# Kernel tuning notes

Hardware: AMD Instinct MI355X
Metric: run time of the kernel (lower is better)

Reference implementation:

```python
import jax, jax.numpy as jnp
import numpy as np

D_MODEL = 512
DFF = 2048
E = 8
K = 2
B, N = 2, 2048


def setup_inputs() -> dict:
    key = jax.random.key(0)
    ks = jax.random.split(key, 6)
    x = jax.random.normal(ks[0], (B, N, D_MODEL), dtype=jnp.float32)
    # router: nn.Linear(d_model, E, bias=False), init normal(std=0.01), weight [E, d]
    router_w = jax.random.normal(ks[1], (E, D_MODEL), dtype=jnp.float32) * 0.01
    # expert linear1.weight [dff, d], linear2.weight [d, dff], xavier-uniform; biases zero in torch init,
    # but use small random biases so the backward test exercises their grads meaningfully.
    lim1 = float(np.sqrt(6.0 / (D_MODEL + DFF)))
    w1_all = jax.random.uniform(ks[2], (E, DFF, D_MODEL), minval=-lim1, maxval=lim1, dtype=jnp.float32)
    w2_all = jax.random.uniform(ks[3], (E, D_MODEL, DFF), minval=-lim1, maxval=lim1, dtype=jnp.float32)
    b1_all = jax.random.normal(ks[4], (E, DFF), dtype=jnp.float32) * 0.01
    b2_all = jax.random.normal(ks[5], (E, D_MODEL), dtype=jnp.float32) * 0.01
    return {"x": x, "router_w": router_w, "w1_all": w1_all, "b1_all": b1_all,
            "w2_all": w2_all, "b2_all": b2_all}


def reference(x, router_w, w1_all, b1_all, w2_all, b2_all):
    Bb, Nn, C = x.shape
    L = Bb * Nn
    x_flat = x.reshape(L, C)

    # Router: logits -> softmax -> top-k -> renormalized weights
    router_logits = x_flat @ router_w.T                      # [L, E]
    router_probs = jax.nn.softmax(router_logits, axis=-1)
    expert_weights, expert_indices = jax.lax.top_k(router_probs, K)  # [L, K]
    expert_weights = expert_weights / (jnp.sum(expert_weights, axis=-1, keepdims=True) + 1e-9)

    # Dense per-expert MLP (same math as per-token gathered bmm; dropout in eval = identity)
    h = jax.nn.relu(jnp.einsum('lc,efc->lef', x_flat, w1_all) + b1_all[None])  # [L, E, dff]
    out_all = jnp.einsum('lef,ecf->lec', h, w2_all) + b2_all[None]             # [L, E, C]

    # Gather selected experts' outputs and combine
    out_sel = jnp.take_along_axis(out_all, expert_indices[:, :, None], axis=1)  # [L, K, C]
    final = jnp.sum(out_sel * expert_weights[:, :, None], axis=1)               # [L, C]
    return final.reshape(Bb, Nn, C)
```

## Files before the change

kernel.cpp:

```cpp
#include <hip/hip_runtime.h>

#define D_MODEL 512
#define DFF 2048
#define NEXP 8
#define LTOK 4096
#define NPAIR 8192
#define PMAX 9216
#define MAXT 72

#define HD_COUNTS 0
#define HD_CURSOR 8
#define HD_OFF    16
#define HD_NTILES 25
#define HD_TILE_E 32
#define HD_TILE_R 112

typedef __attribute__((ext_vector_type(8))) short bf16x8;
typedef __attribute__((ext_vector_type(4))) float f32x4;

__device__ __forceinline__ unsigned short f2bf(float f){
  unsigned u = __builtin_bit_cast(unsigned, f);
  u += 0x7fffu + ((u>>16)&1u);
  return (unsigned short)(u>>16);
}

template<int N> __device__ __forceinline__ void wait_vm(){
  if constexpr (N==6)      asm volatile("s_waitcnt vmcnt(6)" ::: "memory");
  else                     asm volatile("s_waitcnt vmcnt(0)" ::: "memory");
}
#define RAW_BARRIER() asm volatile("s_barrier" ::: "memory")

__global__ void prep_kernel(const float* __restrict__ w1, const float* __restrict__ w2,
                            unsigned short* __restrict__ w1b, unsigned short* __restrict__ w2b,
                            const float* __restrict__ x, const float* __restrict__ rw,
                            int* __restrict__ pair_e, float* __restrict__ pair_w){
  int bx = blockIdx.x;
  int tid = threadIdx.x;
  if (bx < 8192){
    int id = bx*256 + tid;
    const int per = NEXP*DFF*D_MODEL/8;
    const float* src; unsigned short* dst; int k;
    if (id < per){ src = w1; dst = w1b; k = id; }
    else         { src = w2; dst = w2b; k = id - per; }
    const float4* s = (const float4*)(src + (size_t)k*8);
    float4 a = s[0], b = s[1];
    uint4 o;
    o.x = (unsigned)f2bf(a.x) | ((unsigned)f2bf(a.y)<<16);
    o.y = (unsigned)f2bf(a.z) | ((unsigned)f2bf(a.w)<<16);
    o.z = (unsigned)f2bf(b.x) | ((unsigned)f2bf(b.y)<<16);
    o.w = (unsigned)f2bf(b.z) | ((unsigned)f2bf(b.w)<<16);
    *(uint4*)(dst + (size_t)k*8) = o;
  } else {
    int t = (bx - 8192)*4 + (tid>>6);
    int l = tid & 63;
    const float* xr = x + (size_t)t*D_MODEL;
    float xv[8];
    #pragma unroll
    for (int j=0;j<8;j++) xv[j] = xr[j*64+l];
    double lg[NEXP];
    #pragma unroll
    for (int e=0;e<NEXP;e++){
      const float* we = rw + e*D_MODEL;
      double s = 0.0;
      #pragma unroll
      for (int j=0;j<8;j++) s += (double)xv[j] * (double)we[j*64+l];
      #pragma unroll
      for (int off=32; off; off>>=1) s += __shfl_xor(s, off);
      lg[e] = s;
    }
    if (l==0){
      double mx = lg[0];
      #pragma unroll
      for (int e=1;e<NEXP;e++) if (lg[e]>mx) mx = lg[e];
      double p[NEXP], sum = 0.0;
      #pragma unroll
      for (int e=0;e<NEXP;e++){ p[e] = exp(lg[e]-mx); sum += p[e]; }
      #pragma unroll
      for (int e=0;e<NEXP;e++) p[e] /= sum;
      int i0 = 0;
      for (int e=1;e<NEXP;e++) if (p[e] > p[i0]) i0 = e;
      int i1 = (i0==0) ? 1 : 0;
      for (int e=0;e<NEXP;e++){ if (e==i0) continue; if (p[e] > p[i1]) i1 = e; }
      double s2 = p[i0] + p[i1] + 1e-9;
      pair_e[2*t]   = i0;  pair_e[2*t+1] = i1;
      pair_w[2*t]   = (float)(p[i0]/s2);
      pair_w[2*t+1] = (float)(p[i1]/s2);
    }
  }
}

__global__ void count_kernel(const int* __restrict__ pair_e, int* __restrict__ hdr){
  __shared__ int cnt[NEXP];
  int tid = threadIdx.x;
  if (tid < NEXP) cnt[tid] = 0;
  __syncthreads();
  int base = blockIdx.x*1024;
  #pragma unroll
  for (int i=0;i<4;i++) atomicAdd(&cnt[pair_e[base + i*256 + tid]], 1);
  __syncthreads();
  if (tid < NEXP) atomicAdd(&hdr[HD_COUNTS+tid], cnt[tid]);
}

__global__ void plan_kernel(int* __restrict__ hdr, int* __restrict__ gtk){
  if (threadIdx.x==0){
    int off=0, nt=0;
    for (int e=0;e<NEXP;e++){
      hdr[HD_OFF+e]=off;
      int c = hdr[HD_COUNTS+e];
      int tiles = (c+127)>>7;
      for (int i=0;i<tiles;i++){ hdr[HD_TILE_E+nt]=e; hdr[HD_TILE_R+nt]=off+(i<<7); nt++; }
      off += tiles<<7;
    }
    hdr[HD_OFF+NEXP]=off;
    hdr[HD_NTILES]=nt;
  }
  for (int i=threadIdx.x; i<PMAX; i+=blockDim.x) gtk[i]=-1;
}

__global__ void assign_gather_kernel(const int* __restrict__ pair_e, int* __restrict__ hdr,
                                     int* __restrict__ gtk, const float* __restrict__ x,
                                     unsigned short* __restrict__ xg){
  __shared__ int cnt[NEXP];
  __shared__ int base[NEXP];
  __shared__ int rowbuf[256];
  int tid = threadIdx.x;
  if (tid < NEXP) cnt[tid] = 0;
  __syncthreads();
  int id = blockIdx.x*256 + tid;
  int e = pair_e[id];
  int myrank = atomicAdd(&cnt[e], 1);
  __syncthreads();
  if (tid < NEXP) base[tid] = atomicAdd(&hdr[HD_CURSOR+tid], cnt[tid]);
  __syncthreads();
  int row = hdr[HD_OFF+e] + base[e] + myrank;
  gtk[row] = id;
  rowbuf[tid] = row;
  __syncthreads();
  int grp = tid>>6, sub = tid&63;
  int base0 = blockIdx.x*256;
  for (int p = grp; p < 256; p += 4){
    int r = rowbuf[p];
    int t = (base0 + p)>>1;
    const float4* s = (const float4*)(x + (size_t)t*D_MODEL + sub*8);
    float4 a = s[0], b = s[1];
    uint4 o;
    o.x = (unsigned)f2bf(a.x) | ((unsigned)f2bf(a.y)<<16);
    o.y = (unsigned)f2bf(a.z) | ((unsigned)f2bf(a.w)<<16);
    o.z = (unsigned)f2bf(b.x) | ((unsigned)f2bf(b.y)<<16);
    o.w = (unsigned)f2bf(b.z) | ((unsigned)f2bf(b.w)<<16);
    *(uint4*)(xg + (size_t)r*D_MODEL + sub*8) = o;
  }
}

__global__ __launch_bounds__(512,2) void gemm1_k(
    const unsigned short* __restrict__ A,
    const unsigned short* __restrict__ Bw,
    const float* __restrict__ bias,
    unsigned short* __restrict__ outH,
    const int* __restrict__ hdr)
{
  constexpr int NWG = MAXT*8;
  __shared__ __align__(16) unsigned short As[2*128*64];
  __shared__ __align__(16) unsigned short Bs[2*256*64];

  int wg  = blockIdx.x;
  int swz = (wg & 7)*(NWG/8) + (wg >> 3);
  int m   = swz >> 3;
  int n0  = (swz & 7) << 8;

  if (m >= hdr[HD_NTILES]) return;
  int e    = hdr[HD_TILE_E+m];
  int row0 = hdr[HD_TILE_R+m];

  int tid = threadIdx.x;
  int w = tid>>6, l = tid&63;
  int wm = w>>2, wn = w&3;

  const unsigned short* Ag = A  + (size_t)row0*D_MODEL;
  const unsigned short* Bg = Bw + (size_t)e*DFF*D_MODEL + (size_t)n0*D_MODEL;

  f32x4 acc[4][4];
  f32x4 zz = {0.f,0.f,0.f,0.f};
  #pragma unroll
  for (int i=0;i<4;i++)
    #pragma unroll
    for (int j=0;j<4;j++) acc[i][j] = zz;

  int srow = (w<<3) + (l>>3);
  int c8   = l&7;
  char* AsB = (char*)As;
  char* BsB = (char*)Bs;

  auto stage = [&](int b, int kt){
    #pragma unroll
    for (int i=0;i<2;i++){
      int r  = i*64 + srow;
      int sc = (c8 ^ (r&7))*8;
      const unsigned short* ga = Ag + (size_t)r*D_MODEL + kt*64 + sc;
      int ldso = b*16384 + i*8192 + w*1024 + l*16;
      __builtin_amdgcn_global_load_lds((const __attribute__((address_space(1))) void*)ga,
                                       (__attribute__((address_space(3))) void*)(AsB + ldso), 16, 0, 0);
    }
    #pragma unroll
    for (int i=0;i<4;i++){
      int r  = i*64 + srow;
      int sc = (c8 ^ (r&7))*8;
      const unsigned short* gb = Bg + (size_t)r*D_MODEL + kt*64 + sc;
      int ldso = b*32768 + i*8192 + w*1024 + l*16;
      __builtin_amdgcn_global_load_lds((const __attribute__((address_space(1))) void*)gb,
                                       (__attribute__((address_space(3))) void*)(BsB + ldso), 16, 0, 0);
    }
  };

  auto compute = [&](int b){
    #pragma unroll
    for (int kk=0;kk<2;kk++){
      bf16x8 av[4], bv[4];
      #pragma unroll
      for (int mi=0;mi<4;mi++){
        int r  = (wm<<6) + (mi<<4) + (l&15);
        int ch = ((kk<<2) + (l>>4)) ^ (r&7);
        av[mi] = *(const bf16x8*)(AsB + b*16384 + r*128 + ch*16);
      }
      #pragma unroll
      for (int ni=0;ni<4;ni++){
        int r  = (wn<<6) + (ni<<4) + (l&15);
        int ch = ((kk<<2) + (l>>4)) ^ (r&7);
        bv[ni] = *(const bf16x8*)(BsB + b*32768 + r*128 + ch*16);
      }
      #pragma unroll
      for (int mi=0;mi<4;mi++)
        #pragma unroll
        for (int ni=0;ni<4;ni++)
          acc[mi][ni] = __builtin_amdgcn_mfma_f32_16x16x32_bf16(av[mi], bv[ni], acc[mi][ni], 0,0,0);
    }
  };

  stage(0, 0);
  int cur = 0;
  for (int kt=0; kt<D_MODEL/64-1; ++kt){
    stage(cur^1, kt+1);
    wait_vm<6>();
    RAW_BARRIER();
    compute(cur);
    asm volatile("s_waitcnt lgkmcnt(0)" ::: "memory");
    RAW_BARRIER();
    cur ^= 1;
  }
  wait_vm<0>();
  RAW_BARRIER();
  compute(cur);

  int lc = l&15, lq = l>>4;
  #pragma unroll
  for (int ni=0;ni<4;ni++){
    int col = n0 + (wn<<6) + (ni<<4) + lc;
    float bcol = bias[e*DFF + col];
    #pragma unroll
    for (int mi=0;mi<4;mi++){
      int rbase = row0 + (wm<<6) + (mi<<4) + lq*4;
      #pragma unroll
      for (int q=0;q<4;q++){
        float v = acc[mi][ni][q] + bcol;
        v = v>0.f ? v : 0.f;
        outH[(size_t)(rbase+q)*DFF + col] = f2bf(v);
      }
    }
  }
}

__global__ __launch_bounds__(256,3) void gemm2_k(
    const unsigned short* __restrict__ A,
    const unsigned short* __restrict__ Bw,
    const float* __restrict__ bias,
    float* __restrict__ outO,
    const float* __restrict__ pair_w,
    const int* __restrict__ hdr,
    const int* __restrict__ gtk)
{
  constexpr int NWG = 2*MAXT*4;
  __shared__ __align__(16) unsigned short As[2*64*64];
  __shared__ __align__(16) unsigned short Bs[2*128*64];

  int wg  = blockIdx.x;
  int swz = (wg & 7)*(NWG/8) + (wg >> 3);
  int m   = swz >> 2;
  int n0  = (swz & 3) << 7;

  if (m >= 2*hdr[HD_NTILES]) return;
  int e    = hdr[HD_TILE_E+(m>>1)];
  int row0 = hdr[HD_TILE_R+(m>>1)] + ((m&1)<<6);

  int tid = threadIdx.x;
  int w = tid>>6, l = tid&63;

  const unsigned short* Ag = A  + (size_t)row0*DFF;
  const unsigned short* Bg = Bw + (size_t)e*D_MODEL*DFF + (size_t)n0*DFF;

  f32x4 acc[4][2];
  f32x4 zz = {0.f,0.f,0.f,0.f};
  #pragma unroll
  for (int i=0;i<4;i++)
    #pragma unroll
    for (int j=0;j<2;j++) acc[i][j] = zz;

  int srow = (w<<3) + (l>>3);
  int c8   = l&7;
  char* AsB = (char*)As;
  char* BsB = (char*)Bs;

  auto stage = [&](int b, int kt){
    #pragma unroll
    for (int i=0;i<2;i++){
      int r  = i*32 + srow;
      int sc = (c8 ^ (r&7))*8;
      const unsigned short* ga = Ag + (size_t)r*DFF + kt*64 + sc;
      int ldso = b*8192 + i*4096 + w*1024 + l*16;
      __builtin_amdgcn_global_load_lds((const __attribute__((address_space(1))) void*)ga,
                                       (__attribute__((address_space(3))) void*)(AsB + ldso), 16, 0, 0);
    }
    #pragma unroll
    for (int i=0;i<4;i++){
      int r  = i*32 + srow;
      int sc = (c8 ^ (r&7))*8;
      const unsigned short* gb = Bg + (size_t)r*DFF + kt*64 + sc;
      int ldso = b*16384 + i*4096 + w*1024 + l*16;
      __builtin_amdgcn_global_load_lds((const __attribute__((address_space(1))) void*)gb,
                                       (__attribute__((address_space(3))) void*)(BsB + ldso), 16, 0, 0);
    }
  };

  auto compute = [&](int b){
    #pragma unroll
    for (int kk=0;kk<2;kk++){
      bf16x8 av[4], bv[2];
      #pragma unroll
      for (int mi=0;mi<4;mi++){
        int r  = (mi<<4) + (l&15);
        int ch = ((kk<<2) + (l>>4)) ^ (r&7);
        av[mi] = *(const bf16x8*)(AsB + b*8192 + r*128 + ch*16);
      }
      #pragma unroll
      for (int ni=0;ni<2;ni++){
        int r  = (w<<5) + (ni<<4) + (l&15);
        int ch = ((kk<<2) + (l>>4)) ^ (r&7);
        bv[ni] = *(const bf16x8*)(BsB + b*16384 + r*128 + ch*16);
      }
      #pragma unroll
      for (int mi=0;mi<4;mi++)
        #pragma unroll
        for (int ni=0;ni<2;ni++)
          acc[mi][ni] = __builtin_amdgcn_mfma_f32_16x16x32_bf16(av[mi], bv[ni], acc[mi][ni], 0,0,0);
    }
  };

  stage(0, 0);
  int cur = 0;
  for (int kt=0; kt<DFF/64-1; ++kt){
    stage(cur^1, kt+1);
    wait_vm<6>();
    RAW_BARRIER();
    compute(cur);
    asm volatile("s_waitcnt lgkmcnt(0)" ::: "memory");
    RAW_BARRIER();
    cur ^= 1;
  }
  wait_vm<0>();
  RAW_BARRIER();
  compute(cur);

  int lc = l&15, lq = l>>4;
  #pragma unroll
  for (int ni=0;ni<2;ni++){
    int col = n0 + (w<<5) + (ni<<4) + lc;
    float bcol = bias[e*D_MODEL + col];
    #pragma unroll
    for (int mi=0;mi<4;mi++){
      int rbase = row0 + (mi<<4) + lq*4;
      #pragma unroll
      for (int q=0;q<4;q++){
        int gr = rbase + q;
        float v = acc[mi][ni][q] + bcol;
        int tk = gtk[gr];
        if (tk>=0){
          float wgt = pair_w[tk];
          atomicAdd(&outO[(size_t)(tk>>1)*D_MODEL + col], wgt*v);
        }
      }
    }
  }
}

extern "C" void kernel_launch(void* const* d_in, const int* in_sizes, int n_in,
                              void* d_out, int out_size, void* d_ws, size_t ws_size,
                              hipStream_t stream){
  const float* x  = (const float*)d_in[0];
  const float* rw = (const float*)d_in[1];
  const float* w1 = (const float*)d_in[2];
  const float* b1 = (const float*)d_in[3];
  const float* w2 = (const float*)d_in[4];
  const float* b2 = (const float*)d_in[5];
  float* out = (float*)d_out;

  const size_t OFF_HDR  = 0;
  const size_t OFF_PE   = 1024;
  const size_t OFF_PW   = 66560;
  const size_t OFF_GTK  = 99328;
  const size_t OFF_XG   = 180224;
  const size_t OFF_W1B  = OFF_XG  + (size_t)PMAX*D_MODEL*2;
  const size_t OFF_W2B  = OFF_W1B + (size_t)NEXP*DFF*D_MODEL*2;
  const size_t OFF_H    = OFF_W2B + (size_t)NEXP*DFF*D_MODEL*2;
  const size_t WS_NEED  = OFF_H   + (size_t)PMAX*DFF*2;
  if (ws_size < WS_NEED) return;

  char* ws = (char*)d_ws;
  int*   hdr    = (int*)(ws + OFF_HDR);
  int*   pair_e = (int*)(ws + OFF_PE);
  float* pair_w = (float*)(ws + OFF_PW);
  int*   gtk    = (int*)(ws + OFF_GTK);
  unsigned short* xg  = (unsigned short*)(ws + OFF_XG);
  unsigned short* w1b = (unsigned short*)(ws + OFF_W1B);
  unsigned short* w2b = (unsigned short*)(ws + OFF_W2B);
  unsigned short* h   = (unsigned short*)(ws + OFF_H);

  hipMemsetAsync(hdr, 0, 1024, stream);
  hipMemsetAsync(out, 0, (size_t)LTOK*D_MODEL*sizeof(float), stream);
  prep_kernel<<<9216, 256, 0, stream>>>(w1, w2, w1b, w2b, x, rw, pair_e, pair_w);
  count_kernel<<<NPAIR/1024, 256, 0, stream>>>(pair_e, hdr);
  plan_kernel<<<1, 256, 0, stream>>>(hdr, gtk);
  assign_gather_kernel<<<NPAIR/256, 256, 0, stream>>>(pair_e, hdr, gtk, x, xg);
  gemm1_k<<<MAXT*8, 512, 0, stream>>>(xg, w1b, b1, h, hdr);
  gemm2_k<<<2*MAXT*4, 256, 0, stream>>>(h, w2b, b2, out, pair_w, hdr, gtk);
}
```

Baseline: 156.8 us.

## Triple-buffer GEMM K-loop prefetch and split router from weight conversion

```diff
diff --git a/kernel.cpp b/kernel.cpp
--- a/kernel.cpp
+++ b/kernel.cpp
@@ -25,68 +25,66 @@
 }
 
 template<int N> __device__ __forceinline__ void wait_vm(){
-  if constexpr (N==6)      asm volatile("s_waitcnt vmcnt(6)" ::: "memory");
+  if constexpr (N==12)     asm volatile("s_waitcnt vmcnt(12)" ::: "memory");
+  else if constexpr (N==6) asm volatile("s_waitcnt vmcnt(6)" ::: "memory");
   else                     asm volatile("s_waitcnt vmcnt(0)" ::: "memory");
 }
 #define RAW_BARRIER() asm volatile("s_barrier" ::: "memory")
 
-__global__ void prep_kernel(const float* __restrict__ w1, const float* __restrict__ w2,
-                            unsigned short* __restrict__ w1b, unsigned short* __restrict__ w2b,
-                            const float* __restrict__ x, const float* __restrict__ rw,
+__global__ void router_top2(const float* __restrict__ x, const float* __restrict__ rw,
                             int* __restrict__ pair_e, float* __restrict__ pair_w){
-  int bx = blockIdx.x;
-  int tid = threadIdx.x;
-  if (bx < 8192){
-    int id = bx*256 + tid;
-    const int per = NEXP*DFF*D_MODEL/8;
-    const float* src; unsigned short* dst; int k;
-    if (id < per){ src = w1; dst = w1b; k = id; }
-    else         { src = w2; dst = w2b; k = id - per; }
-    const float4* s = (const float4*)(src + (size_t)k*8);
-    float4 a = s[0], b = s[1];
-    uint4 o;
-    o.x = (unsigned)f2bf(a.x) | ((unsigned)f2bf(a.y)<<16);
-    o.y = (unsigned)f2bf(a.z) | ((unsigned)f2bf(a.w)<<16);
-    o.z = (unsigned)f2bf(b.x) | ((unsigned)f2bf(b.y)<<16);
-    o.w = (unsigned)f2bf(b.z) | ((unsigned)f2bf(b.w)<<16);
-    *(uint4*)(dst + (size_t)k*8) = o;
-  } else {
-    int t = (bx - 8192)*4 + (tid>>6);
-    int l = tid & 63;
-    const float* xr = x + (size_t)t*D_MODEL;
-    float xv[8];
-    #pragma unroll
-    for (int j=0;j<8;j++) xv[j] = xr[j*64+l];
-    double lg[NEXP];
-    #pragma unroll
-    for (int e=0;e<NEXP;e++){
-      const float* we = rw + e*D_MODEL;
-      double s = 0.0;
-      #pragma unroll
-      for (int j=0;j<8;j++) s += (double)xv[j] * (double)we[j*64+l];
-      #pragma unroll
-      for (int off=32; off; off>>=1) s += __shfl_xor(s, off);
-      lg[e] = s;
-    }
-    if (l==0){
-      double mx = lg[0];
-      #pragma unroll
-      for (int e=1;e<NEXP;e++) if (lg[e]>mx) mx = lg[e];
-      double p[NEXP], sum = 0.0;
-      #pragma unroll
-      for (int e=0;e<NEXP;e++){ p[e] = exp(lg[e]-mx); sum += p[e]; }
-      #pragma unroll
-      for (int e=0;e<NEXP;e++) p[e] /= sum;
-      int i0 = 0;
-      for (int e=1;e<NEXP;e++) if (p[e] > p[i0]) i0 = e;
-      int i1 = (i0==0) ? 1 : 0;
-      for (int e=0;e<NEXP;e++){ if (e==i0) continue; if (p[e] > p[i1]) i1 = e; }
-      double s2 = p[i0] + p[i1] + 1e-9;
-      pair_e[2*t]   = i0;  pair_e[2*t+1] = i1;
-      pair_w[2*t]   = (float)(p[i0]/s2);
-      pair_w[2*t+1] = (float)(p[i1]/s2);
-    }
-  }
+  int t = blockIdx.x;
+  int l = threadIdx.x;
+  const float* xr = x + (size_t)t*D_MODEL;
+  float xv[8];
+  #pragma unroll
+  for (int j=0;j<8;j++) xv[j] = xr[j*64+l];
+  double lg[NEXP];
+  #pragma unroll
+  for (int e=0;e<NEXP;e++){
+    const float* we = rw + e*D_MODEL;
+    double s = 0.0;
+    #pragma unroll
+    for (int j=0;j<8;j++) s += (double)xv[j] * (double)we[j*64+l];
+    #pragma unroll
+    for (int off=32; off; off>>=1) s += __shfl_xor(s, off);
+    lg[e] = s;
+  }
+  if (l==0){
+    double mx = lg[0];
+    #pragma unroll
+    for (int e=1;e<NEXP;e++) if (lg[e]>mx) mx = lg[e];
+    double p[NEXP], sum = 0.0;
+    #pragma unroll
+    for (int e=0;e<NEXP;e++){ p[e] = exp(lg[e]-mx); sum += p[e]; }
+    #pragma unroll
+    for (int e=0;e<NEXP;e++) p[e] /= sum;
+    int i0 = 0;
+    for (int e=1;e<NEXP;e++) if (p[e] > p[i0]) i0 = e;
+    int i1 = (i0==0) ? 1 : 0;
+    for (int e=0;e<NEXP;e++){ if (e==i0) continue; if (p[e] > p[i1]) i1 = e; }
+    double s2 = p[i0] + p[i1] + 1e-9;
+    pair_e[2*t]   = i0;  pair_e[2*t+1] = i1;
+    pair_w[2*t]   = (float)(p[i0]/s2);
+    pair_w[2*t+1] = (float)(p[i1]/s2);
+  }
+}
+
+__global__ void convw_kernel(const float* __restrict__ w1, const float* __restrict__ w2,
+                             unsigned short* __restrict__ w1b, unsigned short* __restrict__ w2b){
+  int id = blockIdx.x*256 + threadIdx.x;
+  const int per = NEXP*DFF*D_MODEL/8;
+  const float* src; unsigned short* dst; int k;
+  if (id < per){ src = w1; dst = w1b; k = id; }
+  else         { src = w2; dst = w2b; k = id - per; }
+  const float4* s = (const float4*)(src + (size_t)k*8);
+  float4 a = s[0], b = s[1];
+  uint4 o;
+  o.x = (unsigned)f2bf(a.x) | ((unsigned)f2bf(a.y)<<16);
+  o.y = (unsigned)f2bf(a.z) | ((unsigned)f2bf(a.w)<<16);
+  o.z = (unsigned)f2bf(b.x) | ((unsigned)f2bf(b.y)<<16);
+  o.w = (unsigned)f2bf(b.z) | ((unsigned)f2bf(b.w)<<16);
+  *(uint4*)(dst + (size_t)k*8) = o;
 }
 
 __global__ void count_kernel(const int* __restrict__ pair_e, int* __restrict__ hdr){
@@ -160,8 +158,9 @@
     const int* __restrict__ hdr)
 {
   constexpr int NWG = MAXT*8;
-  __shared__ __align__(16) unsigned short As[2*128*64];
-  __shared__ __align__(16) unsigned short Bs[2*256*64];
+  constexpr int NTK = D_MODEL/64;
+  __shared__ __align__(16) unsigned short As[3*128*64];
+  __shared__ __align__(16) unsigned short Bs[3*256*64];
 
   int wg  = blockIdx.x;
   int swz = (wg & 7)*(NWG/8) + (wg >> 3);
@@ -236,20 +235,18 @@
     }
   };
 
-  stage(0, 0);
-  int cur = 0;
-  for (int kt=0; kt<D_MODEL/64-1; ++kt){
-    stage(cur^1, kt+1);
-    wait_vm<6>();
+  stage(0,0); stage(1,1); stage(2,2);
+  for (int t=0; t<NTK; ++t){
+    if (t < NTK-2)       wait_vm<12>();
+    else if (t == NTK-2) wait_vm<6>();
+    else                 wait_vm<0>();
     RAW_BARRIER();
-    compute(cur);
+    int b = t%3;
+    compute(b);
     asm volatile("s_waitcnt lgkmcnt(0)" ::: "memory");
     RAW_BARRIER();
-    cur ^= 1;
-  }
-  wait_vm<0>();
-  RAW_BARRIER();
-  compute(cur);
+    if (t+3 < NTK) stage(b, t+3);
+  }
 
   int lc = l&15, lq = l>>4;
   #pragma unroll
@@ -269,7 +266,7 @@
   }
 }
 
-__global__ __launch_bounds__(256,3) void gemm2_k(
+__global__ __launch_bounds__(256,2) void gemm2_k(
     const unsigned short* __restrict__ A,
     const unsigned short* __restrict__ Bw,
     const float* __restrict__ bias,
@@ -279,8 +276,9 @@
     const int* __restrict__ gtk)
 {
   constexpr int NWG = 2*MAXT*4;
-  __shared__ __align__(16) unsigned short As[2*64*64];
-  __shared__ __align__(16) unsigned short Bs[2*128*64];
+  constexpr int NTK = DFF/64;
+  __shared__ __align__(16) unsigned short As[3*64*64];
+  __shared__ __align__(16) unsigned short Bs[3*128*64];
 
   int wg  = blockIdx.x;
   int swz = (wg & 7)*(NWG/8) + (wg >> 3);
@@ -354,20 +352,18 @@
     }
   };
 
-  stage(0, 0);
-  int cur = 0;
-  for (int kt=0; kt<DFF/64-1; ++kt){
-    stage(cur^1, kt+1);
-    wait_vm<6>();
+  stage(0,0); stage(1,1); stage(2,2);
+  for (int t=0; t<NTK; ++t){
+    if (t < NTK-2)       wait_vm<12>();
+    else if (t == NTK-2) wait_vm<6>();
+    else                 wait_vm<0>();
     RAW_BARRIER();
-    compute(cur);
+    int b = t%3;
+    compute(b);
     asm volatile("s_waitcnt lgkmcnt(0)" ::: "memory");
     RAW_BARRIER();
-    cur ^= 1;
-  }
-  wait_vm<0>();
-  RAW_BARRIER();
-  compute(cur);
+    if (t+3 < NTK) stage(b, t+3);
+  }
 
   int lc = l&15, lq = l>>4;
   #pragma unroll
@@ -425,7 +421,8 @@
 
   hipMemsetAsync(hdr, 0, 1024, stream);
   hipMemsetAsync(out, 0, (size_t)LTOK*D_MODEL*sizeof(float), stream);
-  prep_kernel<<<9216, 256, 0, stream>>>(w1, w2, w1b, w2b, x, rw, pair_e, pair_w);
+  router_top2<<<LTOK, 64, 0, stream>>>(x, rw, pair_e, pair_w);
+  convw_kernel<<<8192, 256, 0, stream>>>(w1, w2, w1b, w2b);
   count_kernel<<<NPAIR/1024, 256, 0, stream>>>(pair_e, hdr);
   plan_kernel<<<1, 256, 0, stream>>>(hdr, gtk);
   assign_gather_kernel<<<NPAIR/256, 256, 0, stream>>>(pair_e, hdr, gtk, x, xg);
```

Result: slower. 185.4 us (+18.2%).

## Enlarge expert row tiles to 256 and split-K gemm2 across wave groups

Applied to the files above, without the earlier changes.

```diff
diff --git a/kernel.cpp b/kernel.cpp
--- a/kernel.cpp
+++ b/kernel.cpp
@@ -5,8 +5,8 @@
 #define NEXP 8
 #define LTOK 4096
 #define NPAIR 8192
-#define PMAX 9216
-#define MAXT 72
+#define PMAX2 10240
+#define MAXT2 40
 
 #define HD_COUNTS 0
 #define HD_CURSOR 8
@@ -25,68 +25,66 @@
 }
 
 template<int N> __device__ __forceinline__ void wait_vm(){
-  if constexpr (N==6)      asm volatile("s_waitcnt vmcnt(6)" ::: "memory");
+  if constexpr (N==8)      asm volatile("s_waitcnt vmcnt(8)" ::: "memory");
+  else if constexpr (N==6) asm volatile("s_waitcnt vmcnt(6)" ::: "memory");
   else                     asm volatile("s_waitcnt vmcnt(0)" ::: "memory");
 }
 #define RAW_BARRIER() asm volatile("s_barrier" ::: "memory")
 
-__global__ void prep_kernel(const float* __restrict__ w1, const float* __restrict__ w2,
-                            unsigned short* __restrict__ w1b, unsigned short* __restrict__ w2b,
-                            const float* __restrict__ x, const float* __restrict__ rw,
+__global__ void router_top2(const float* __restrict__ x, const float* __restrict__ rw,
                             int* __restrict__ pair_e, float* __restrict__ pair_w){
-  int bx = blockIdx.x;
-  int tid = threadIdx.x;
-  if (bx < 8192){
-    int id = bx*256 + tid;
-    const int per = NEXP*DFF*D_MODEL/8;
-    const float* src; unsigned short* dst; int k;
-    if (id < per){ src = w1; dst = w1b; k = id; }
-    else         { src = w2; dst = w2b; k = id - per; }
-    const float4* s = (const float4*)(src + (size_t)k*8);
-    float4 a = s[0], b = s[1];
-    uint4 o;
-    o.x = (unsigned)f2bf(a.x) | ((unsigned)f2bf(a.y)<<16);
-    o.y = (unsigned)f2bf(a.z) | ((unsigned)f2bf(a.w)<<16);
-    o.z = (unsigned)f2bf(b.x) | ((unsigned)f2bf(b.y)<<16);
-    o.w = (unsigned)f2bf(b.z) | ((unsigned)f2bf(b.w)<<16);
-    *(uint4*)(dst + (size_t)k*8) = o;
-  } else {
-    int t = (bx - 8192)*4 + (tid>>6);
-    int l = tid & 63;
-    const float* xr = x + (size_t)t*D_MODEL;
-    float xv[8];
-    #pragma unroll
-    for (int j=0;j<8;j++) xv[j] = xr[j*64+l];
-    double lg[NEXP];
-    #pragma unroll
-    for (int e=0;e<NEXP;e++){
-      const float* we = rw + e*D_MODEL;
-      double s = 0.0;
-      #pragma unroll
-      for (int j=0;j<8;j++) s += (double)xv[j] * (double)we[j*64+l];
-      #pragma unroll
-      for (int off=32; off; off>>=1) s += __shfl_xor(s, off);
-      lg[e] = s;
-    }
-    if (l==0){
-      double mx = lg[0];
-      #pragma unroll
-      for (int e=1;e<NEXP;e++) if (lg[e]>mx) mx = lg[e];
-      double p[NEXP], sum = 0.0;
-      #pragma unroll
-      for (int e=0;e<NEXP;e++){ p[e] = exp(lg[e]-mx); sum += p[e]; }
-      #pragma unroll
-      for (int e=0;e<NEXP;e++) p[e] /= sum;
-      int i0 = 0;
-      for (int e=1;e<NEXP;e++) if (p[e] > p[i0]) i0 = e;
-      int i1 = (i0==0) ? 1 : 0;
-      for (int e=0;e<NEXP;e++){ if (e==i0) continue; if (p[e] > p[i1]) i1 = e; }
-      double s2 = p[i0] + p[i1] + 1e-9;
-      pair_e[2*t]   = i0;  pair_e[2*t+1] = i1;
-      pair_w[2*t]   = (float)(p[i0]/s2);
-      pair_w[2*t+1] = (float)(p[i1]/s2);
-    }
-  }
+  int t = blockIdx.x;
+  int l = threadIdx.x;
+  const float* xr = x + (size_t)t*D_MODEL;
+  float xv[8];
+  #pragma unroll
+  for (int j=0;j<8;j++) xv[j] = xr[j*64+l];
+  double lg[NEXP];
+  #pragma unroll
+  for (int e=0;e<NEXP;e++){
+    const float* we = rw + e*D_MODEL;
+    double s = 0.0;
+    #pragma unroll
+    for (int j=0;j<8;j++) s += (double)xv[j] * (double)we[j*64+l];
+    #pragma unroll
+    for (int off=32; off; off>>=1) s += __shfl_xor(s, off);
+    lg[e] = s;
+  }
+  if (l==0){
+    double mx = lg[0];
+    #pragma unroll
+    for (int e=1;e<NEXP;e++) if (lg[e]>mx) mx = lg[e];
+    double p[NEXP], sum = 0.0;
+    #pragma unroll
+    for (int e=0;e<NEXP;e++){ p[e] = exp(lg[e]-mx); sum += p[e]; }
+    #pragma unroll
+    for (int e=0;e<NEXP;e++) p[e] /= sum;
+    int i0 = 0;
+    for (int e=1;e<NEXP;e++) if (p[e] > p[i0]) i0 = e;
+    int i1 = (i0==0) ? 1 : 0;
+    for (int e=0;e<NEXP;e++){ if (e==i0) continue; if (p[e] > p[i1]) i1 = e; }
+    double s2 = p[i0] + p[i1] + 1e-9;
+    pair_e[2*t]   = i0;  pair_e[2*t+1] = i1;
+    pair_w[2*t]   = (float)(p[i0]/s2);
+    pair_w[2*t+1] = (float)(p[i1]/s2);
+  }
+}
+
+__global__ void convw_kernel(const float* __restrict__ w1, const float* __restrict__ w2,
+                             unsigned short* __restrict__ w1b, unsigned short* __restrict__ w2b){
+  int id = blockIdx.x*256 + threadIdx.x;
+  const int per = NEXP*DFF*D_MODEL/8;
+  const float* src; unsigned short* dst; int k;
+  if (id < per){ src = w1; dst = w1b; k = id; }
+  else         { src = w2; dst = w2b; k = id - per; }
+  const float4* s = (const float4*)(src + (size_t)k*8);
+  float4 a = s[0], b = s[1];
+  uint4 o;
+  o.x = (unsigned)f2bf(a.x) | ((unsigned)f2bf(a.y)<<16);
+  o.y = (unsigned)f2bf(a.z) | ((unsigned)f2bf(a.w)<<16);
+  o.z = (unsigned)f2bf(b.x) | ((unsigned)f2bf(b.y)<<16);
+  o.w = (unsigned)f2bf(b.z) | ((unsigned)f2bf(b.w)<<16);
+  *(uint4*)(dst + (size_t)k*8) = o;
 }
 
 __global__ void count_kernel(const int* __restrict__ pair_e, int* __restrict__ hdr){
@@ -107,14 +105,14 @@
     for (int e=0;e<NEXP;e++){
       hdr[HD_OFF+e]=off;
       int c = hdr[HD_COUNTS+e];
-      int tiles = (c+127)>>7;
-      for (int i=0;i<tiles;i++){ hdr[HD_TILE_E+nt]=e; hdr[HD_TILE_R+nt]=off+(i<<7); nt++; }
-      off += tiles<<7;
+      int tiles = (c+255)>>8;
+      for (int i=0;i<tiles;i++){ hdr[HD_TILE_E+nt]=e; hdr[HD_TILE_R+nt]=off+(i<<8); nt++; }
+      off += tiles<<8;
     }
     hdr[HD_OFF+NEXP]=off;
     hdr[HD_NTILES]=nt;
   }
-  for (int i=threadIdx.x; i<PMAX; i+=blockDim.x) gtk[i]=-1;
+  for (int i=threadIdx.x; i<PMAX2; i+=blockDim.x) gtk[i]=-1;
 }
 
 __global__ void assign_gather_kernel(const int* __restrict__ pair_e, int* __restrict__ hdr,
@@ -159,8 +157,9 @@
     unsigned short* __restrict__ outH,
     const int* __restrict__ hdr)
 {
-  constexpr int NWG = MAXT*8;
-  __shared__ __align__(16) unsigned short As[2*128*64];
+  constexpr int NWG = MAXT2*8;
+  constexpr int NTK = D_MODEL/64;
+  __shared__ __align__(16) unsigned short As[2*256*64];
   __shared__ __align__(16) unsigned short Bs[2*256*64];
 
   int wg  = blockIdx.x;
@@ -179,25 +178,25 @@
   const unsigned short* Ag = A  + (size_t)row0*D_MODEL;
   const unsigned short* Bg = Bw + (size_t)e*DFF*D_MODEL + (size_t)n0*D_MODEL;
 
-  f32x4 acc[4][4];
+  f32x4 acc[8][4];
   f32x4 zz = {0.f,0.f,0.f,0.f};
   #pragma unroll
-  for (int i=0;i<4;i++)
+  for (int i=0;i<8;i++)
     #pragma unroll
     for (int j=0;j<4;j++) acc[i][j] = zz;
 
-  int srow = (w<<3) + (l>>3);
-  int c8   = l&7;
+  int srow = tid>>3;
+  int c8   = tid&7;
   char* AsB = (char*)As;
   char* BsB = (char*)Bs;
 
   auto stage = [&](int b, int kt){
     #pragma unroll
-    for (int i=0;i<2;i++){
+    for (int i=0;i<4;i++){
       int r  = i*64 + srow;
       int sc = (c8 ^ (r&7))*8;
       const unsigned short* ga = Ag + (size_t)r*D_MODEL + kt*64 + sc;
-      int ldso = b*16384 + i*8192 + w*1024 + l*16;
+      int ldso = b*32768 + i*8192 + tid*16;
       __builtin_amdgcn_global_load_lds((const __attribute__((address_space(1))) void*)ga,
                                        (__attribute__((address_space(3))) void*)(AsB + ldso), 16, 0, 0);
     }
@@ -206,7 +205,7 @@
       int r  = i*64 + srow;
       int sc = (c8 ^ (r&7))*8;
       const unsigned short* gb = Bg + (size_t)r*D_MODEL + kt*64 + sc;
-      int ldso = b*32768 + i*8192 + w*1024 + l*16;
+      int ldso = b*32768 + i*8192 + tid*16;
       __builtin_amdgcn_global_load_lds((const __attribute__((address_space(1))) void*)gb,
                                        (__attribute__((address_space(3))) void*)(BsB + ldso), 16, 0, 0);
     }
@@ -215,12 +214,12 @@
   auto compute = [&](int b){
     #pragma unroll
     for (int kk=0;kk<2;kk++){
-      bf16x8 av[4], bv[4];
-      #pragma unroll
-      for (int mi=0;mi<4;mi++){
-        int r  = (wm<<6) + (mi<<4) + (l&15);
+      bf16x8 av[8], bv[4];
+      #pragma unroll
+      for (int mi=0;mi<8;mi++){
+        int r  = (wm<<7) + (mi<<4) + (l&15);
         int ch = ((kk<<2) + (l>>4)) ^ (r&7);
-        av[mi] = *(const bf16x8*)(AsB + b*16384 + r*128 + ch*16);
+        av[mi] = *(const bf16x8*)(AsB + b*32768 + r*128 + ch*16);
       }
       #pragma unroll
       for (int ni=0;ni<4;ni++){
@@ -229,7 +228,7 @@
         bv[ni] = *(const bf16x8*)(BsB + b*32768 + r*128 + ch*16);
       }
       #pragma unroll
-      for (int mi=0;mi<4;mi++)
+      for (int mi=0;mi<8;mi++)
         #pragma unroll
         for (int ni=0;ni<4;ni++)
           acc[mi][ni] = __builtin_amdgcn_mfma_f32_16x16x32_bf16(av[mi], bv[ni], acc[mi][ni], 0,0,0);
@@ -238,9 +237,9 @@
 
   stage(0, 0);
   int cur = 0;
-  for (int kt=0; kt<D_MODEL/64-1; ++kt){
+  for (int kt=0; kt<NTK-1; ++kt){
     stage(cur^1, kt+1);
-    wait_vm<6>();
+    wait_vm<8>();
     RAW_BARRIER();
     compute(cur);
     asm volatile("s_waitcnt lgkmcnt(0)" ::: "memory");
@@ -257,8 +256,8 @@
     int col = n0 + (wn<<6) + (ni<<4) + lc;
     float bcol = bias[e*DFF + col];
     #pragma unroll
-    for (int mi=0;mi<4;mi++){
-      int rbase = row0 + (wm<<6) + (mi<<4) + lq*4;
+    for (int mi=0;mi<8;mi++){
+      int rbase = row0 + (wm<<7) + (mi<<4) + lq*4;
       #pragma unroll
       for (int q=0;q<4;q++){
         float v = acc[mi][ni][q] + bcol;
@@ -269,7 +268,7 @@
   }
 }
 
-__global__ __launch_bounds__(256,3) void gemm2_k(
+__global__ __launch_bounds__(512,2) void gemm2_k(
     const unsigned short* __restrict__ A,
     const unsigned short* __restrict__ Bw,
     const float* __restrict__ bias,
@@ -278,85 +277,88 @@
     const int* __restrict__ hdr,
     const int* __restrict__ gtk)
 {
-  constexpr int NWG = 2*MAXT*4;
-  __shared__ __align__(16) unsigned short As[2*64*64];
+  constexpr int NWG = MAXT2*4*2;
+  constexpr int NTK = 16;
+  __shared__ __align__(16) unsigned short As[2*256*64];
   __shared__ __align__(16) unsigned short Bs[2*128*64];
 
   int wg  = blockIdx.x;
   int swz = (wg & 7)*(NWG/8) + (wg >> 3);
-  int m   = swz >> 2;
-  int n0  = (swz & 3) << 7;
-
-  if (m >= 2*hdr[HD_NTILES]) return;
-  int e    = hdr[HD_TILE_E+(m>>1)];
-  int row0 = hdr[HD_TILE_R+(m>>1)] + ((m&1)<<6);
+  int m   = swz >> 3;
+  int nt  = (swz >> 1) & 3;
+  int kh  = swz & 1;
+
+  if (m >= hdr[HD_NTILES]) return;
+  int e    = hdr[HD_TILE_E+m];
+  int row0 = hdr[HD_TILE_R+m];
+  int n0   = nt << 7;
 
   int tid = threadIdx.x;
   int w = tid>>6, l = tid&63;
-
-  const unsigned short* Ag = A  + (size_t)row0*DFF;
-  const unsigned short* Bg = Bw + (size_t)e*D_MODEL*DFF + (size_t)n0*DFF;
-
-  f32x4 acc[4][2];
+  int kkw  = w>>2;
+  int slot = w&3;
+  int wm = slot>>1, wn = slot&1;
+
+  const unsigned short* Ag = A  + (size_t)row0*DFF + (size_t)kh*1024;
+  const unsigned short* Bg = Bw + (size_t)e*D_MODEL*DFF + (size_t)n0*DFF + (size_t)kh*1024;
+
+  f32x4 acc[8][4];
   f32x4 zz = {0.f,0.f,0.f,0.f};
   #pragma unroll
-  for (int i=0;i<4;i++)
-    #pragma unroll
-    for (int j=0;j<2;j++) acc[i][j] = zz;
-
-  int srow = (w<<3) + (l>>3);
-  int c8   = l&7;
+  for (int i=0;i<8;i++)
+    #pragma unroll
+    for (int j=0;j<4;j++) acc[i][j] = zz;
+
+  int srow = tid>>3;
+  int c8   = tid&7;
   char* AsB = (char*)As;
   char* BsB = (char*)Bs;
 
   auto stage = [&](int b, int kt){
     #pragma unroll
-    for (int i=0;i<2;i++){
-      int r  = i*32 + srow;
+    for (int i=0;i<4;i++){
+      int r  = i*64 + srow;
       int sc = (c8 ^ (r&7))*8;
       const unsigned short* ga = Ag + (size_t)r*DFF + kt*64 + sc;
-      int ldso = b*8192 + i*4096 + w*1024 + l*16;
+      int ldso = b*32768 + i*8192 + tid*16;
       __builtin_amdgcn_global_load_lds((const __attribute__((address_space(1))) void*)ga,
                                        (__attribute__((address_space(3))) void*)(AsB + ldso), 16, 0, 0);
     }
     #pragma unroll
-    for (int i=0;i<4;i++){
-      int r  = i*32 + srow;
+    for (int i=0;i<2;i++){
+      int r  = i*64 + srow;
       int sc = (c8 ^ (r&7))*8;
       const unsigned short* gb = Bg + (size_t)r*DFF + kt*64 + sc;
-      int ldso = b*16384 + i*4096 + w*1024 + l*16;
+      int ldso = b*16384 + i*8192 + tid*16;
       __builtin_amdgcn_global_load_lds((const __attribute__((address_space(1))) void*)gb,
                                        (__attribute__((address_space(3))) void*)(BsB + ldso), 16, 0, 0);
     }
   };
 
   auto compute = [&](int b){
-    #pragma unroll
-    for (int kk=0;kk<2;kk++){
-      bf16x8 av[4], bv[2];
-      #pragma unroll
-      for (int mi=0;mi<4;mi++){
-        int r  = (mi<<4) + (l&15);
-        int ch = ((kk<<2) + (l>>4)) ^ (r&7);
-        av[mi] = *(const bf16x8*)(AsB + b*8192 + r*128 + ch*16);
-      }
-      #pragma unroll
-      for (int ni=0;ni<2;ni++){
-        int r  = (w<<5) + (ni<<4) + (l&15);
-        int ch = ((kk<<2) + (l>>4)) ^ (r&7);
-        bv[ni] = *(const bf16x8*)(BsB + b*16384 + r*128 + ch*16);
-      }
-      #pragma unroll
-      for (int mi=0;mi<4;mi++)
-        #pragma unroll
-        for (int ni=0;ni<2;ni++)
-          acc[mi][ni] = __builtin_amdgcn_mfma_f32_16x16x32_bf16(av[mi], bv[ni], acc[mi][ni], 0,0,0);
-    }
+    bf16x8 av[8], bv[4];
+    #pragma unroll
+    for (int mi=0;mi<8;mi++){
+      int r  = (wm<<7) + (mi<<4) + (l&15);
+      int ch = ((kkw<<2) + (l>>4)) ^ (r&7);
+      av[mi] = *(const bf16x8*)(AsB + b*32768 + r*128 + ch*16);
+    }
+    #pragma unroll
+    for (int ni=0;ni<4;ni++){
+      int r  = (wn<<6) + (ni<<4) + (l&15);
+      int ch = ((kkw<<2) + (l>>4)) ^ (r&7);
+      bv[ni] = *(const bf16x8*)(BsB + b*16384 + r*128 + ch*16);
+    }
+    #pragma unroll
+    for (int mi=0;mi<8;mi++)
+      #pragma unroll
+      for (int ni=0;ni<4;ni++)
+        acc[mi][ni] = __builtin_amdgcn_mfma_f32_16x16x32_bf16(av[mi], bv[ni], acc[mi][ni], 0,0,0);
   };
 
   stage(0, 0);
   int cur = 0;
-  for (int kt=0; kt<DFF/64-1; ++kt){
+  for (int kt=0; kt<NTK-1; ++kt){
     stage(cur^1, kt+1);
     wait_vm<6>();
     RAW_BARRIER();
@@ -370,13 +372,14 @@
   compute(cur);
 
   int lc = l&15, lq = l>>4;
-  #pragma unroll
-  for (int ni=0;ni<2;ni++){
-    int col = n0 + (w<<5) + (ni<<4) + lc;
-    float bcol = bias[e*D_MODEL + col];
-    #pragma unroll
-    for (int mi=0;mi<4;mi++){
-      int rbase = row0 + (mi<<4) + lq*4;
+  bool addb = (kh==0) && (kkw==0);
+  #pragma unroll
+  for (int ni=0;ni<4;ni++){
+    int col = n0 + (wn<<6) + (ni<<4) + lc;
+    float bcol = addb ? bias[e*D_MODEL + col] : 0.f;
+    #pragma unroll
+    for (int mi=0;mi<8;mi++){
+      int rbase = row0 + (wm<<7) + (mi<<4) + lq*4;
       #pragma unroll
       for (int q=0;q<4;q++){
         int gr = rbase + q;
@@ -407,10 +410,10 @@
   const size_t OFF_PW   = 66560;
   const size_t OFF_GTK  = 99328;
   const size_t OFF_XG   = 180224;
-  const size_t OFF_W1B  = OFF_XG  + (size_t)PMAX*D_MODEL*2;
+  const size_t OFF_W1B  = OFF_XG  + (size_t)PMAX2*D_MODEL*2;
   const size_t OFF_W2B  = OFF_W1B + (size_t)NEXP*DFF*D_MODEL*2;
   const size_t OFF_H    = OFF_W2B + (size_t)NEXP*DFF*D_MODEL*2;
-  const size_t WS_NEED  = OFF_H   + (size_t)PMAX*DFF*2;
+  const size_t WS_NEED  = OFF_H   + (size_t)PMAX2*DFF*2;
   if (ws_size < WS_NEED) return;
 
   char* ws = (char*)d_ws;
@@ -425,10 +428,11 @@
 
   hipMemsetAsync(hdr, 0, 1024, stream);
   hipMemsetAsync(out, 0, (size_t)LTOK*D_MODEL*sizeof(float), stream);
-  prep_kernel<<<9216, 256, 0, stream>>>(w1, w2, w1b, w2b, x, rw, pair_e, pair_w);
+  router_top2<<<LTOK, 64, 0, stream>>>(x, rw, pair_e, pair_w);
+  convw_kernel<<<8192, 256, 0, stream>>>(w1, w2, w1b, w2b);
   count_kernel<<<NPAIR/1024, 256, 0, stream>>>(pair_e, hdr);
   plan_kernel<<<1, 256, 0, stream>>>(hdr, gtk);
   assign_gather_kernel<<<NPAIR/256, 256, 0, stream>>>(pair_e, hdr, gtk, x, xg);
-  gemm1_k<<<MAXT*8, 512, 0, stream>>>(xg, w1b, b1, h, hdr);
-  gemm2_k<<<2*MAXT*4, 256, 0, stream>>>(h, w2b, b2, out, pair_w, hdr, gtk);
-}
+  gemm1_k<<<MAXT2*8, 512, 0, stream>>>(xg, w1b, b1, h, hdr);
+  gemm2_k<<<MAXT2*8, 512, 0, stream>>>(h, w2b, b2, out, pair_w, hdr, gtk);
+}
```

Measured after the change: 264.4 us. +68.6%, slower.
